# Performance work log

Hardware: AMD Instinct MI355X
Metric: run time of the kernel (lower is better)

Reference implementation:

```python
import jax, jax.numpy as jnp
import numpy as np

N, E = 100000, 3200000
F_IN, HID, NCLS = 1433, 8, 7
H1, H2 = 8, 1
NEG_SLOPE = 0.2


def gat_layer(x, W, att_src, att_dst, bias, src, dst, heads, ch):
    n = x.shape[0]
    h = (x @ W).reshape(n, heads, ch)                      # [N,H,C]
    a_s = (h * att_src).sum(-1)                            # [N,H]
    a_d = (h * att_dst).sum(-1)                            # [N,H]
    e = a_s[src] + a_d[dst]                                # [Etot,H]
    e = jnp.where(e > 0, e, NEG_SLOPE * e)                 # leaky_relu(0.2)
    m = jax.ops.segment_max(e, dst, num_segments=n)        # per-dst max
    e = jnp.exp(e - m[dst])
    denom = jax.ops.segment_sum(e, dst, num_segments=n)
    alpha = e / (denom[dst] + 1e-16)                       # segment softmax
    msg = h[src] * alpha[:, :, None]                       # [Etot,H,C]
    out = jax.ops.segment_sum(msg, dst, num_segments=n)    # [N,H,C]
    return out.mean(axis=1) + bias                         # concat=False -> head mean


def setup_inputs() -> dict:
    key = jax.random.key(0)
    ks = jax.random.split(key, 10)
    x = jax.random.normal(ks[0], (N, F_IN), dtype=jnp.float32)
    edge_index = jax.random.randint(ks[1], (2, E), 0, N, dtype=jnp.int32)
    s = 0.1
    W1 = jax.random.normal(ks[2], (F_IN, H1 * HID), dtype=jnp.float32) * s
    att_src1 = jax.random.normal(ks[3], (H1, HID), dtype=jnp.float32) * s
    att_dst1 = jax.random.normal(ks[4], (H1, HID), dtype=jnp.float32) * s
    b1 = jnp.zeros((HID,), dtype=jnp.float32)
    W2 = jax.random.normal(ks[5], (HID, H2 * NCLS), dtype=jnp.float32) * s
    att_src2 = jax.random.normal(ks[6], (H2, NCLS), dtype=jnp.float32) * s
    att_dst2 = jax.random.normal(ks[7], (H2, NCLS), dtype=jnp.float32) * s
    b2 = jnp.zeros((NCLS,), dtype=jnp.float32)
    return {"x": x, "edge_index": edge_index, "W1": W1, "att_src1": att_src1,
            "att_dst1": att_dst1, "b1": b1, "W2": W2, "att_src2": att_src2,
            "att_dst2": att_dst2, "b2": b2}


def reference(x, edge_index, W1, att_src1, att_dst1, b1, W2, att_src2, att_dst2, b2):
    n = x.shape[0]
    loops = jnp.arange(n, dtype=edge_index.dtype)
    src = jnp.concatenate([edge_index[0], loops])  # PyG add_self_loops=True
    dst = jnp.concatenate([edge_index[1], loops])
    h = jax.nn.elu(gat_layer(x, W1, att_src1, att_dst1, b1, src, dst, H1, HID))
    out = gat_layer(h, W2, att_src2, att_dst2, b2, src, dst, H2, NCLS)
    return jax.nn.log_softmax(out, axis=-1)
```

## Files before the change

### kernel.cpp

```cpp
#include <hip/hip_runtime.h>

#define N_NODES 100000
#define E_EDGES 3200000
#define F_IN    1433
#define K_PAD   1472
#define NCH     98
#define KPH     64
#define GEMM_BLOCKS 1563

typedef _Float16 f16x4 __attribute__((ext_vector_type(4)));
typedef _Float16 f16x8 __attribute__((ext_vector_type(8)));
typedef float    f32x4 __attribute__((ext_vector_type(4)));

__device__ __forceinline__ void gload_lds16(const void* g, void* l) {
    __builtin_amdgcn_global_load_lds(
        (const __attribute__((address_space(1))) unsigned int*)g,
        (__attribute__((address_space(3))) unsigned int*)l, 16, 0, 0);
}

__global__ void k_init(const float* __restrict__ w1, _Float16* __restrict__ w1t,
                       int* __restrict__ counts) {
    int i = blockIdx.x * 256 + threadIdx.x;
    if (i < N_NODES) counts[i] = 0;
    if (i < 64 * K_PAD) {
        int n = i / K_PAD, k = i - n * K_PAD;
        float v = (k < F_IN) ? w1[(size_t)k * 64 + n] : 0.f;
        w1t[i] = (_Float16)v;
    }
}

__global__ void k_hist(const int* __restrict__ dst, int* __restrict__ counts) {
    int idx = blockIdx.x * 256 + threadIdx.x;
    int4 d4 = ((const int4*)dst)[idx];
    atomicAdd(&counts[d4.x], 1);
    atomicAdd(&counts[d4.y], 1);
    atomicAdd(&counts[d4.z], 1);
    atomicAdd(&counts[d4.w], 1);
}

__global__ void k_scan_a(const int* __restrict__ counts, int* __restrict__ csum) {
    __shared__ int sh[256];
    int b = blockIdx.x, t = threadIdx.x;
    int s = 0;
    for (int j = 0; j < 4; ++j) {
        int idx = b * 1024 + j * 256 + t;
        if (idx < N_NODES) s += counts[idx];
    }
    sh[t] = s; __syncthreads();
    for (int off = 128; off > 0; off >>= 1) {
        if (t < off) sh[t] += sh[t + off];
        __syncthreads();
    }
    if (t == 0) csum[b] = sh[0];
}

__global__ void k_scan_b(int* __restrict__ csum) {
    __shared__ int sh[128];
    int t = threadIdx.x;
    int v = (t < NCH) ? csum[t] : 0;
    sh[t] = v; __syncthreads();
    for (int off = 1; off < 128; off <<= 1) {
        int u = (t >= off) ? sh[t - off] : 0;
        __syncthreads();
        sh[t] += u;
        __syncthreads();
    }
    if (t < NCH) csum[t] = sh[t] - v;
}

__global__ void k_scan_c(const int* __restrict__ counts, const int* __restrict__ csum,
                         int* __restrict__ offsets, int* __restrict__ cursor) {
    __shared__ int sh[256];
    int b = blockIdx.x, t = threadIdx.x;
    int base = b * 1024 + t * 4;
    int c0 = (base + 0 < N_NODES) ? counts[base + 0] : 0;
    int c1 = (base + 1 < N_NODES) ? counts[base + 1] : 0;
    int c2 = (base + 2 < N_NODES) ? counts[base + 2] : 0;
    int c3 = (base + 3 < N_NODES) ? counts[base + 3] : 0;
    int tot = c0 + c1 + c2 + c3;
    sh[t] = tot; __syncthreads();
    for (int off = 1; off < 256; off <<= 1) {
        int v = (t >= off) ? sh[t - off] : 0;
        __syncthreads();
        sh[t] += v;
        __syncthreads();
    }
    int excl = sh[t] - tot;
    int o = csum[b] + excl;
    if (base + 0 < N_NODES) { offsets[base + 0] = o;            cursor[base + 0] = o; }
    if (base + 1 < N_NODES) { int q = o + c0;      offsets[base + 1] = q; cursor[base + 1] = q; }
    if (base + 2 < N_NODES) { int q = o + c0 + c1; offsets[base + 2] = q; cursor[base + 2] = q; }
    if (base + 3 < N_NODES) { int q = o + c0 + c1 + c2; offsets[base + 3] = q; cursor[base + 3] = q; }
}

__global__ __launch_bounds__(256) void k_gemm_scat(const float* __restrict__ x,
                                                   const _Float16* __restrict__ w1t,
                                                   const float* __restrict__ att_src1,
                                                   const float* __restrict__ att_dst1,
                                                   _Float16* __restrict__ h1,
                                                   float* __restrict__ a_s1,
                                                   float* __restrict__ a_d1,
                                                   const int* __restrict__ src,
                                                   const int* __restrict__ dst,
                                                   int* __restrict__ cursor,
                                                   int* __restrict__ sorted_src) {
    __shared__ __align__(16) char AsB[2][64 * 256];
    __shared__ __align__(16) char BsB[2][64 * 128];
    const int tid = threadIdx.x;

    if (blockIdx.x >= GEMM_BLOCKS) {
        int idx = (blockIdx.x - GEMM_BLOCKS) * 256 + tid;
        int4 s4 = ((const int4*)src)[idx];
        int4 d4 = ((const int4*)dst)[idx];
        int p;
        p = atomicAdd(&cursor[d4.x], 1); sorted_src[p] = s4.x;
        p = atomicAdd(&cursor[d4.y], 1); sorted_src[p] = s4.y;
        p = atomicAdd(&cursor[d4.z], 1); sorted_src[p] = s4.z;
        p = atomicAdd(&cursor[d4.w], 1); sorted_src[p] = s4.w;
        return;
    }

    const int lane = tid & 63;
    const int wave = tid >> 6;
    const int l16  = lane & 15;
    const int l4   = lane >> 4;
    const int brow0 = blockIdx.x * 64;

    f32x4 acc[4] = {};

    auto stageA = [&](int buf, int ph) {
        #pragma unroll
        for (int j = 0; j < 4; ++j) {
            int p = j * 256 + tid;
            int row = p >> 4, q = p & 15;
            int qs = q ^ (row & 7);
            int grow = brow0 + row; if (grow > N_NODES - 1) grow = N_NODES - 1;
            const float* gp = x + (size_t)grow * F_IN + ph * KPH + qs * 4;
            gload_lds16(gp, AsB[buf] + j * 4096 + wave * 1024);
        }
    };
    auto stageB = [&](int buf, int ph) {
        #pragma unroll
        for (int j = 0; j < 2; ++j) {
            int p = j * 256 + tid;
            int col = p >> 3, c = p & 7;
            int cs = c ^ (col & 7);
            const _Float16* gp = w1t + (size_t)col * K_PAD + ph * KPH + cs * 8;
            gload_lds16(gp, BsB[buf] + j * 4096 + wave * 1024);
        }
    };
    auto stageTailA = [&](int buf) {
        for (int i = tid; i < 1024; i += 256) {
            int row = i >> 4, q = i & 15;
            int qs = q ^ (row & 7);
            int grow = brow0 + row; if (grow > N_NODES - 1) grow = N_NODES - 1;
            const float* gp = x + (size_t)grow * F_IN;
            float4 v;
            #pragma unroll
            for (int jj = 0; jj < 4; ++jj) {
                int k = 1408 + qs * 4 + jj;
                ((float*)&v)[jj] = (k < F_IN) ? gp[k] : 0.f;
            }
            *(float4*)(AsB[buf] + row * 256 + q * 16) = v;
        }
    };
    auto compute = [&](int buf) {
        const int rA = wave * 16 + l16;
        const char* Ab = AsB[buf] + rA * 256;
        const int r7 = rA & 7;
        #pragma unroll
        for (int st = 0; st < 4; ++st) {
            float4 af = *(const float4*)(Ab + ((((st << 2) + l4) ^ r7) << 4));
            f16x4 a = { (_Float16)af.x, (_Float16)af.y, (_Float16)af.z, (_Float16)af.w };
            #pragma unroll
            for (int t = 0; t < 4; ++t) {
                const int cB = t * 16 + l16;
                const int chunk = (st << 1) + (l4 >> 1);
                const int boff = cB * 128 + ((chunk ^ (cB & 7)) << 4) + ((l4 & 1) << 3);
                f16x4 b = *(const f16x4*)(BsB[buf] + boff);
                acc[t] = __builtin_amdgcn_mfma_f32_16x16x16f16(a, b, acc[t], 0, 0, 0);
            }
        }
    };

    stageA(0, 0); stageB(0, 0);
    __syncthreads();
    int cur = 0;
    for (int ph = 0; ph < 22; ++ph) {
        if (ph + 1 < 22) { stageA(cur ^ 1, ph + 1); stageB(cur ^ 1, ph + 1); }
        else             { stageTailA(cur ^ 1);     stageB(cur ^ 1, 22);     }
        compute(cur);
        __syncthreads();
        cur ^= 1;
    }
    compute(cur);

    const int wrow0 = brow0 + wave * 16;
    #pragma unroll
    for (int t = 0; t < 4; ++t) {
        const int head = t * 2 + (l16 >> 3);
        const int ch   = l16 & 7;
        const float asc = att_src1[head * 8 + ch];
        const float adc = att_dst1[head * 8 + ch];
        #pragma unroll
        for (int j = 0; j < 4; ++j) {
            int r = wrow0 + l4 * 4 + j;
            float ps = acc[t][j] * asc, pd = acc[t][j] * adc;
            ps += __shfl_xor(ps, 1); ps += __shfl_xor(ps, 2); ps += __shfl_xor(ps, 4);
            pd += __shfl_xor(pd, 1); pd += __shfl_xor(pd, 2); pd += __shfl_xor(pd, 4);
            if (r < N_NODES) {
                h1[(size_t)r * 64 + t * 16 + l16] = (_Float16)acc[t][j];
                if (ch == 0) {
                    a_s1[r * 8 + head] = ps;
                    a_d1[r * 8 + head] = pd;
                }
            }
        }
    }
}

__global__ __launch_bounds__(256) void k_agg1(
    const int* __restrict__ offsets, const int* __restrict__ counts,
    const int* __restrict__ sorted_src,
    const float* __restrict__ a_s1, const float* __restrict__ a_d1,
    const _Float16* __restrict__ h1, const float* __restrict__ b1,
    const float* __restrict__ w2, const float* __restrict__ att_src2,
    const float* __restrict__ att_dst2,
    _Float16* __restrict__ g, float* __restrict__ a_s2, float* __restrict__ a_d2) {
    const int lane = threadIdx.x & 63;
    const int wave = threadIdx.x >> 6;
    const int h    = lane & 7;
    const int es   = lane >> 3;
    const int n    = blockIdx.x * 4 + wave;
    const int start = offsets[n];
    const int cnt   = counts[n];
    const float adn = a_d1[n * 8 + h];
    float et = a_s1[n * 8 + h] + adn;
    const float e_self = et > 0.f ? et : 0.2f * et;

    float m = e_self, denom = 0.f;
    float acc[8] = {0.f,0.f,0.f,0.f,0.f,0.f,0.f,0.f};
    if (es == 0) {
        denom = 1.f;
        f16x8 hv0 = *(const f16x8*)(h1 + (size_t)n * 64 + h * 8);
        #pragma unroll
        for (int c = 0; c < 8; ++c) acc[c] = (float)hv0[c];
    }
    for (int i = es; i < cnt; i += 32) {
        const int i1 = i + 8, i2 = i + 16, i3 = i + 24;
        const bool b1v = i1 < cnt, b2v = i2 < cnt, b3v = i3 < cnt;
        int s0 = sorted_src[start + i];
        int s1 = sorted_src[start + (b1v ? i1 : i)];
        int s2 = sorted_src[start + (b2v ? i2 : i)];
        int s3 = sorted_src[start + (b3v ? i3 : i)];
        float a0 = a_s1[s0 * 8 + h];
        float a1 = a_s1[s1 * 8 + h];
        float a2 = a_s1[s2 * 8 + h];
        float a3 = a_s1[s3 * 8 + h];
        f16x8 v0 = *(const f16x8*)(h1 + (size_t)s0 * 64 + h * 8);
        f16x8 v1 = *(const f16x8*)(h1 + (size_t)s1 * 64 + h * 8);
        f16x8 v2 = *(const f16x8*)(h1 + (size_t)s2 * 64 + h * 8);
        f16x8 v3 = *(const f16x8*)(h1 + (size_t)s3 * 64 + h * 8);
        {
            float e = a0 + adn; e = e > 0.f ? e : 0.2f * e;
            if (e > m + 8.f) { float sc = __expf(m - e); denom *= sc;
                #pragma unroll
                for (int c = 0; c < 8; ++c) acc[c] *= sc; m = e; }
            float p = __expf(e - m); denom += p;
            #pragma unroll
            for (int c = 0; c < 8; ++c) acc[c] += p * (float)v0[c];
        }
        if (b1v) {
            float e = a1 + adn; e = e > 0.f ? e : 0.2f * e;
            if (e > m + 8.f) { float sc = __expf(m - e); denom *= sc;
                #pragma unroll
                for (int c = 0; c < 8; ++c) acc[c] *= sc; m = e; }
            float p = __expf(e - m); denom += p;
            #pragma unroll
            for (int c = 0; c < 8; ++c) acc[c] += p * (float)v1[c];
        }
        if (b2v) {
            float e = a2 + adn; e = e > 0.f ? e : 0.2f * e;
            if (e > m + 8.f) { float sc = __expf(m - e); denom *= sc;
                #pragma unroll
                for (int c = 0; c < 8; ++c) acc[c] *= sc; m = e; }
            float p = __expf(e - m); denom += p;
            #pragma unroll
            for (int c = 0; c < 8; ++c) acc[c] += p * (float)v2[c];
        }
        if (b3v) {
            float e = a3 + adn; e = e > 0.f ? e : 0.2f * e;
            if (e > m + 8.f) { float sc = __expf(m - e); denom *= sc;
                #pragma unroll
                for (int c = 0; c < 8; ++c) acc[c] *= sc; m = e; }
            float p = __expf(e - m); denom += p;
            #pragma unroll
            for (int c = 0; c < 8; ++c) acc[c] += p * (float)v3[c];
        }
    }
    #pragma unroll
    for (int d = 8; d < 64; d <<= 1) {
        float mo = __shfl_xor(m, d);
        float dn = __shfl_xor(denom, d);
        float mn = fmaxf(m, mo);
        float sa = __expf(m - mn), sb = __expf(mo - mn);
        denom = denom * sa + dn * sb;
        #pragma unroll
        for (int c = 0; c < 8; ++c) {
            float ao = __shfl_xor(acc[c], d);
            acc[c] = acc[c] * sa + ao * sb;
        }
        m = mn;
    }
    float inv = 1.f / (denom + 1e-16f);
    float hc[8];
    #pragma unroll
    for (int c = 0; c < 8; ++c) {
        float v = acc[c] * inv;
        v += __shfl_xor(v, 1);
        v += __shfl_xor(v, 2);
        v += __shfl_xor(v, 4);
        float o = 0.125f * v + b1[c];
        hc[c] = o > 0.f ? o : expm1f(o);
    }
    if (lane == 0) {
        float s2 = 0.f, d2 = 0.f;
        f16x8 gr;
        #pragma unroll
        for (int j = 0; j < 7; ++j) {
            float t = 0.f;
            #pragma unroll
            for (int c = 0; c < 8; ++c) t += hc[c] * w2[c * 7 + j];
            gr[j] = (_Float16)t;
            s2 += t * att_src2[j];
            d2 += t * att_dst2[j];
        }
        gr[7] = (_Float16)0.f;
        *(f16x8*)(g + (size_t)n * 8) = gr;
        a_s2[n] = s2;
        a_d2[n] = d2;
    }
}

__global__ __launch_bounds__(256) void k_agg2(
    const int* __restrict__ offsets, const int* __restrict__ counts,
    const int* __restrict__ sorted_src,
    const float* __restrict__ a_s2, const float* __restrict__ a_d2,
    const _Float16* __restrict__ g, const float* __restrict__ b2,
    float* __restrict__ outp) {
    const int tid  = threadIdx.x;
    const int lane = tid & 63;
    const int wave = tid >> 6;
    const int grp  = lane >> 3;
    const int s    = lane & 7;
    const int n    = blockIdx.x * 32 + wave * 8 + grp;
    const int start = offsets[n];
    const int cnt   = counts[n];
    const float adn = a_d2[n];
    float et = a_s2[n] + adn;
    const float e_self = et > 0.f ? et : 0.2f * et;

    float m = e_self, denom = 0.f;
    float acc[8] = {0.f,0.f,0.f,0.f,0.f,0.f,0.f,0.f};
    if (s == 0) {
        denom = 1.f;
        f16x8 gv0 = *(const f16x8*)(g + (size_t)n * 8);
        #pragma unroll
        for (int c = 0; c < 8; ++c) acc[c] = (float)gv0[c];
    }
    for (int i = s; i < cnt; i += 32) {
        const int i1 = i + 8, i2 = i + 16, i3 = i + 24;
        const bool b1v = i1 < cnt, b2v = i2 < cnt, b3v = i3 < cnt;
        int s0 = sorted_src[start + i];
        int s1 = sorted_src[start + (b1v ? i1 : i)];
        int s2 = sorted_src[start + (b2v ? i2 : i)];
        int s3 = sorted_src[start + (b3v ? i3 : i)];
        float a0 = a_s2[s0], a1 = a_s2[s1], a2 = a_s2[s2], a3 = a_s2[s3];
        f16x8 v0 = *(const f16x8*)(g + (size_t)s0 * 8);
        f16x8 v1 = *(const f16x8*)(g + (size_t)s1 * 8);
        f16x8 v2 = *(const f16x8*)(g + (size_t)s2 * 8);
        f16x8 v3 = *(const f16x8*)(g + (size_t)s3 * 8);
        {
            float e = a0 + adn; e = e > 0.f ? e : 0.2f * e;
            if (e > m + 8.f) { float sc = __expf(m - e); denom *= sc;
                #pragma unroll
                for (int c = 0; c < 8; ++c) acc[c] *= sc; m = e; }
            float p = __expf(e - m); denom += p;
            #pragma unroll
            for (int c = 0; c < 8; ++c) acc[c] += p * (float)v0[c];
        }
        if (b1v) {
            float e = a1 + adn; e = e > 0.f ? e : 0.2f * e;
            if (e > m + 8.f) { float sc = __expf(m - e); denom *= sc;
                #pragma unroll
                for (int c = 0; c < 8; ++c) acc[c] *= sc; m = e; }
            float p = __expf(e - m); denom += p;
            #pragma unroll
            for (int c = 0; c < 8; ++c) acc[c] += p * (float)v1[c];
        }
        if (b2v) {
            float e = a2 + adn; e = e > 0.f ? e : 0.2f * e;
            if (e > m + 8.f) { float sc = __expf(m - e); denom *= sc;
                #pragma unroll
                for (int c = 0; c < 8; ++c) acc[c] *= sc; m = e; }
            float p = __expf(e - m); denom += p;
            #pragma unroll
            for (int c = 0; c < 8; ++c) acc[c] += p * (float)v2[c];
        }
        if (b3v) {
            float e = a3 + adn; e = e > 0.f ? e : 0.2f * e;
            if (e > m + 8.f) { float sc = __expf(m - e); denom *= sc;
                #pragma unroll
                for (int c = 0; c < 8; ++c) acc[c] *= sc; m = e; }
            float p = __expf(e - m); denom += p;
            #pragma unroll
            for (int c = 0; c < 8; ++c) acc[c] += p * (float)v3[c];
        }
    }
    #pragma unroll
    for (int d = 1; d < 8; d <<= 1) {
        float mo = __shfl_xor(m, d, 8);
        float dn = __shfl_xor(denom, d, 8);
        float mn = fmaxf(m, mo);
        float sa = __expf(m - mn), sb = __expf(mo - mn);
        denom = denom * sa + dn * sb;
        #pragma unroll
        for (int c = 0; c < 8; ++c) {
            float ao = __shfl_xor(acc[c], d, 8);
            acc[c] = acc[c] * sa + ao * sb;
        }
        m = mn;
    }
    float inv = 1.f / (denom + 1e-16f);
    float o[7]; float mx = -1e30f;
    #pragma unroll
    for (int c = 0; c < 7; ++c) { o[c] = acc[c] * inv + b2[c]; mx = fmaxf(mx, o[c]); }
    float se = 0.f;
    #pragma unroll
    for (int c = 0; c < 7; ++c) se += __expf(o[c] - mx);
    float ls = mx + logf(se);
    if (s < 7) outp[n * 7 + s] = o[s] - ls;
}

extern "C" void kernel_launch(void* const* d_in, const int* in_sizes, int n_in,
                              void* d_out, int out_size, void* d_ws, size_t ws_size,
                              hipStream_t stream) {
    const float* x        = (const float*)d_in[0];
    const int*   ei       = (const int*)d_in[1];
    const float* W1       = (const float*)d_in[2];
    const float* att_src1 = (const float*)d_in[3];
    const float* att_dst1 = (const float*)d_in[4];
    const float* b1       = (const float*)d_in[5];
    const float* W2       = (const float*)d_in[6];
    const float* att_src2 = (const float*)d_in[7];
    const float* att_dst2 = (const float*)d_in[8];
    const float* b2       = (const float*)d_in[9];
    const int* src = ei;
    const int* dst = ei + E_EDGES;

    char* ws = (char*)d_ws;
    size_t off = 0;
    auto alloc = [&](size_t bytes) -> char* {
        char* p = ws + off;
        off = (off + bytes + 255) & ~(size_t)255;
        return p;
    };
    _Float16* h1         = (_Float16*)alloc((size_t)N_NODES * 64 * 2);
    float*    a_s1       = (float*)   alloc((size_t)N_NODES * 8 * 4);
    float*    a_d1       = (float*)   alloc((size_t)N_NODES * 8 * 4);
    _Float16* w1t        = (_Float16*)alloc((size_t)64 * K_PAD * 2);
    int*      counts     = (int*)     alloc((size_t)N_NODES * 4);
    int*      offsets    = (int*)     alloc((size_t)N_NODES * 4);
    int*      cursor     = (int*)     alloc((size_t)N_NODES * 4);
    int*      csum       = (int*)     alloc((size_t)NCH * 4);
    int*      sorted_src = (int*)     alloc((size_t)(E_EDGES + 32) * 4);
    _Float16* gbuf       = (_Float16*)alloc((size_t)N_NODES * 8 * 2);
    float*    a_s2       = (float*)   alloc((size_t)N_NODES * 4);
    float*    a_d2       = (float*)   alloc((size_t)N_NODES * 4);
    float*    outp       = (float*)d_out;

    hipLaunchKernelGGL(k_init,      dim3(391),   dim3(256), 0, stream, W1, w1t, counts);
    hipLaunchKernelGGL(k_hist,      dim3(3125),  dim3(256), 0, stream, dst, counts);
    hipLaunchKernelGGL(k_scan_a,    dim3(NCH),   dim3(256), 0, stream, counts, csum);
    hipLaunchKernelGGL(k_scan_b,    dim3(1),     dim3(128), 0, stream, csum);
    hipLaunchKernelGGL(k_scan_c,    dim3(NCH),   dim3(256), 0, stream, counts, csum, offsets, cursor);
    hipLaunchKernelGGL(k_gemm_scat, dim3(GEMM_BLOCKS + 3125), dim3(256), 0, stream,
                       x, w1t, att_src1, att_dst1, h1, a_s1, a_d1,
                       src, dst, cursor, sorted_src);
    hipLaunchKernelGGL(k_agg1,      dim3(25000), dim3(256), 0, stream, offsets, counts, sorted_src,
                       a_s1, a_d1, h1, b1, W2, att_src2, att_dst2, gbuf, a_s2, a_d2);
    hipLaunchKernelGGL(k_agg2,      dim3(3125),  dim3(256), 0, stream, offsets, counts, sorted_src,
                       a_s2, a_d2, gbuf, b2, outp);
}
```

Baseline: 569.0 us.

## Interleave scatter blocks with GEMM blocks and prefetch two K-phases ahead

Result: faster. 541.8 us (-4.8%).

```diff
diff --git a/kernel.cpp b/kernel.cpp
--- a/kernel.cpp
+++ b/kernel.cpp
@@ -6,7 +6,6 @@
 #define K_PAD   1472
 #define NCH     98
 #define KPH     64
-#define GEMM_BLOCKS 1563
 
 typedef _Float16 f16x4 __attribute__((ext_vector_type(4)));
 typedef _Float16 f16x8 __attribute__((ext_vector_type(8)));
@@ -108,23 +107,30 @@
     __shared__ __align__(16) char BsB[2][64 * 128];
     const int tid = threadIdx.x;
 
-    if (blockIdx.x >= GEMM_BLOCKS) {
-        int idx = (blockIdx.x - GEMM_BLOCKS) * 256 + tid;
-        int4 s4 = ((const int4*)src)[idx];
-        int4 d4 = ((const int4*)dst)[idx];
-        int p;
-        p = atomicAdd(&cursor[d4.x], 1); sorted_src[p] = s4.x;
-        p = atomicAdd(&cursor[d4.y], 1); sorted_src[p] = s4.y;
-        p = atomicAdd(&cursor[d4.z], 1); sorted_src[p] = s4.z;
-        p = atomicAdd(&cursor[d4.w], 1); sorted_src[p] = s4.w;
+    if (blockIdx.x & 1) {
+        const int sid = blockIdx.x >> 1;
+        #pragma unroll
+        for (int rep = 0; rep < 2; ++rep) {
+            int i4 = sid * 512 + rep * 256 + tid;
+            if (i4 < E_EDGES / 4) {
+                int4 s4 = ((const int4*)src)[i4];
+                int4 d4 = ((const int4*)dst)[i4];
+                int p;
+                p = atomicAdd(&cursor[d4.x], 1); sorted_src[p] = s4.x;
+                p = atomicAdd(&cursor[d4.y], 1); sorted_src[p] = s4.y;
+                p = atomicAdd(&cursor[d4.z], 1); sorted_src[p] = s4.z;
+                p = atomicAdd(&cursor[d4.w], 1); sorted_src[p] = s4.w;
+            }
+        }
         return;
     }
 
+    const int gid  = blockIdx.x >> 1;
     const int lane = tid & 63;
     const int wave = tid >> 6;
     const int l16  = lane & 15;
     const int l4   = lane >> 4;
-    const int brow0 = blockIdx.x * 64;
+    const int brow0 = gid * 64;
 
     f32x4 acc[4] = {};
 
@@ -184,16 +190,23 @@
     };
 
     stageA(0, 0); stageB(0, 0);
-    __syncthreads();
-    int cur = 0;
-    for (int ph = 0; ph < 22; ++ph) {
-        if (ph + 1 < 22) { stageA(cur ^ 1, ph + 1); stageB(cur ^ 1, ph + 1); }
-        else             { stageTailA(cur ^ 1);     stageB(cur ^ 1, 22);     }
-        compute(cur);
-        __syncthreads();
-        cur ^= 1;
-    }
-    compute(cur);
+    stageA(1, 1); stageB(1, 1);
+    for (int ph = 0; ph <= 20; ++ph) {
+        asm volatile("s_waitcnt vmcnt(6)" ::: "memory");
+        __builtin_amdgcn_sched_barrier(0);
+        __builtin_amdgcn_s_barrier();
+        compute(ph & 1);
+        asm volatile("s_waitcnt lgkmcnt(0)" ::: "memory");
+        __builtin_amdgcn_s_barrier();
+        int nxt = ph + 2;
+        if (nxt < 22)       { stageA(ph & 1, nxt); stageB(ph & 1, nxt); }
+        else if (nxt == 22) { stageTailA(ph & 1);  stageB(ph & 1, 22);  }
+    }
+    asm volatile("s_waitcnt vmcnt(0) lgkmcnt(0)" ::: "memory");
+    __builtin_amdgcn_sched_barrier(0);
+    __builtin_amdgcn_s_barrier();
+    compute(1);
+    compute(0);
 
     const int wrow0 = brow0 + wave * 16;
     #pragma unroll
@@ -484,7 +497,7 @@
     hipLaunchKernelGGL(k_scan_a,    dim3(NCH),   dim3(256), 0, stream, counts, csum);
     hipLaunchKernelGGL(k_scan_b,    dim3(1),     dim3(128), 0, stream, csum);
     hipLaunchKernelGGL(k_scan_c,    dim3(NCH),   dim3(256), 0, stream, counts, csum, offsets, cursor);
-    hipLaunchKernelGGL(k_gemm_scat, dim3(GEMM_BLOCKS + 3125), dim3(256), 0, stream,
+    hipLaunchKernelGGL(k_gemm_scat, dim3(3126),  dim3(256), 0, stream,
                        x, w1t, att_src1, att_dst1, h1, a_s1, a_d1,
                        src, dst, cursor, sorted_src);
     hipLaunchKernelGGL(k_agg1,      dim3(25000), dim3(256), 0, stream, offsets, counts, sorted_src,
```
